# Optimization experiments

Hardware: AMD Instinct MI355X
Metric: run time of the kernel (lower is better)

Reference implementation:

```python
import jax, jax.numpy as jnp
import numpy as np

TAU = 2.0          # LIF membrane time constant (spikingjelly default)
ALPHA = 2.0        # ATan surrogate width
EPS = 1e-5         # BatchNorm eps
NUM_HEADS = 8
SCALE = 0.125

@jax.custom_vjp
def spike(x):
    return (x >= 0.0).astype(x.dtype)

def _spike_fwd(x):
    return (x >= 0.0).astype(x.dtype), x

def _spike_bwd(x, g):
    # ATan surrogate gradient (spikingjelly default)
    return (g * (ALPHA / 2.0) / (1.0 + (jnp.pi / 2.0 * ALPHA * x) ** 2),)

spike.defvjp(_spike_fwd, _spike_bwd)

def lif(x, v_th):
    # Multi-step LIF over leading time axis T; hard reset to 0, v_reset=0.
    def step(v, xt):
        h = v + (xt - v) / TAU
        s = spike(h - v_th)
        return h * (1.0 - s), s
    _, s = jax.lax.scan(step, jnp.zeros_like(x[0]), x)
    return s

def bn(x, g, b, m, v):
    # BatchNorm1d in eval mode over channel (last) dim
    return (x - m) * jax.lax.rsqrt(v + EPS) * g + b

def setup_inputs() -> dict:
    key = jax.random.key(0)
    ks = jax.random.split(key, 16)
    T, B, N, C = 4, 16, 512, 512
    s = 1.0 / np.sqrt(C)
    inp = {"x": jax.random.normal(ks[0], (T, B, N, C), jnp.float32)}
    for i, p in enumerate("qkvp"):
        inp[f"w{p}"] = jax.random.normal(ks[1 + i], (C, C), jnp.float32) * s
        inp[f"b{p}"] = jnp.zeros((C,), jnp.float32)
        inp[f"{p}_gamma"] = jnp.ones((C,), jnp.float32)
        inp[f"{p}_beta"] = jnp.zeros((C,), jnp.float32)
        inp[f"{p}_mean"] = jax.random.normal(ks[5 + i], (C,), jnp.float32) * 0.1
        inp[f"{p}_var"] = jax.random.uniform(ks[9 + i], (C,), jnp.float32, minval=0.5, maxval=1.5)
    return inp

def reference(x, wq, bq, q_gamma, q_beta, q_mean, q_var,
              wk, bk, k_gamma, k_beta, k_mean, k_var,
              wv, bv, v_gamma, v_beta, v_mean, v_var,
              wp, bp, p_gamma, p_beta, p_mean, p_var):
    T, B, N, C = x.shape
    H = NUM_HEADS
    D = C // H

    def branch(w, b, g, be, m, va):
        y = bn(x @ w.T + b, g, be, m, va)          # Linear -> BN1d (eval)
        y = lif(y, 1.0)                             # spiking activation
        return y.reshape(T, B, N, H, D).transpose(0, 1, 3, 2, 4)  # [T,B,H,N,D]

    q = branch(wq, bq, q_gamma, q_beta, q_mean, q_var)
    k = branch(wk, bk, k_gamma, k_beta, k_mean, k_var)
    v = branch(wv, bv, v_gamma, v_beta, v_mean, v_var)

    attn = jnp.einsum('tbhnd,tbhmd->tbhnm', q, k) * SCALE  # [T,B,H,N,N]
    o = jnp.einsum('tbhnm,tbhmd->tbhnd', attn, v)          # [T,B,H,N,D]
    o = o.transpose(0, 1, 3, 2, 4).reshape(T, B, N, C)
    o = lif(o, 0.5)                                        # attn_lif, v_th=0.5
    o = bn(o @ wp.T + bp, p_gamma, p_beta, p_mean, p_var)
    return lif(o, 1.0)
```

## Files before the change

### kernel.cpp

```cpp
#include <hip/hip_runtime.h>
#include <hip/hip_bf16.h>
#include <hip/hip_fp16.h>
#include <cstddef>
#include <cstdint>

#define T_ 4
#define B_ 16
#define N_ 512
#define C_ 512
#define H_ 8
#define D_ 64
#define BN_T (B_*N_)

typedef unsigned short u16;
typedef __attribute__((ext_vector_type(8))) short bf16x8;
typedef __attribute__((ext_vector_type(8))) _Float16 f16x8;
typedef __attribute__((ext_vector_type(8))) unsigned short u16x8;
typedef __attribute__((ext_vector_type(4))) float f32x4;

__device__ __forceinline__ u16 f2bf_exact(float f) {
    union { float f; unsigned u; } x; x.f = f; return (u16)(x.u >> 16);
}
__device__ __forceinline__ void split2(float f, u16& h1, u16& h2) {
    const __half a = __float2half(f);
    const float r = (f - __half2float(a)) * 2048.0f;
    const __half b = __float2half(r);
    h1 = __half_as_ushort(a); h2 = __half_as_ushort(b);
}
__device__ __forceinline__ int swz(int rr, int q) {
    return (rr << 6) + (((q ^ ((rr >> 1) & 3)) & 3) << 4);
}
__device__ __forceinline__ int SW(int row, int col) {
    return (row << 6) + (col ^ ((row & 7) << 3));
}
__device__ __forceinline__ void gload16(const void* g, void* l) {
    __builtin_amdgcn_global_load_lds(
        (const __attribute__((address_space(1))) unsigned int*)g,
        (__attribute__((address_space(3))) unsigned int*)l, 16, 0, 0);
}

__global__ __launch_bounds__(256) void k_split_x(
    const float* __restrict__ x, u16* __restrict__ x1t, u16* __restrict__ x2t)
{
    const int tile = blockIdx.x;
    const int mt = tile >> 4, kb = tile & 15;
    const int tid = threadIdx.x;
    const int rr = tid >> 1, kh = tid & 1;
    const int t = rr & 3, bn = mt * 32 + (rr >> 2);
    const float* src = x + ((size_t)t * BN_T + bn) * C_ + kb * 32 + kh * 16;
    float f[16];
    *reinterpret_cast<float4*>(f + 0)  = *reinterpret_cast<const float4*>(src + 0);
    *reinterpret_cast<float4*>(f + 4)  = *reinterpret_cast<const float4*>(src + 4);
    *reinterpret_cast<float4*>(f + 8)  = *reinterpret_cast<const float4*>(src + 8);
    *reinterpret_cast<float4*>(f + 12) = *reinterpret_cast<const float4*>(src + 12);
    char* d1 = (char*)(x1t + ((size_t)tile << 12));
    char* d2 = (char*)(x2t + ((size_t)tile << 12));
    #pragma unroll
    for (int j = 0; j < 2; ++j) {
        u16x8 p1, p2;
        #pragma unroll
        for (int e = 0; e < 8; ++e) { u16 h1, h2; split2(f[8*j+e], h1, h2); p1[e] = h1; p2[e] = h2; }
        const int q = 2 * kh + j;
        *reinterpret_cast<u16x8*>(d1 + swz(rr, q)) = p1;
        *reinterpret_cast<u16x8*>(d2 + swz(rr, q)) = p2;
    }
}

__global__ __launch_bounds__(256) void k_split_w(
    const float* __restrict__ w, u16* __restrict__ w1t, u16* __restrict__ w2t)
{
    const int tile = blockIdx.x;
    const int nt = tile >> 4, kb = tile & 15;
    const int tid = threadIdx.x;
    const int rr = tid >> 1, kh = tid & 1;
    const int c = nt * 128 + rr;
    const float* src = w + (size_t)c * C_ + kb * 32 + kh * 16;
    float f[16];
    *reinterpret_cast<float4*>(f + 0)  = *reinterpret_cast<const float4*>(src + 0);
    *reinterpret_cast<float4*>(f + 4)  = *reinterpret_cast<const float4*>(src + 4);
    *reinterpret_cast<float4*>(f + 8)  = *reinterpret_cast<const float4*>(src + 8);
    *reinterpret_cast<float4*>(f + 12) = *reinterpret_cast<const float4*>(src + 12);
    char* d1 = (char*)(w1t + ((size_t)tile << 12));
    char* d2 = (char*)(w2t + ((size_t)tile << 12));
    #pragma unroll
    for (int j = 0; j < 2; ++j) {
        u16x8 p1, p2;
        #pragma unroll
        for (int e = 0; e < 8; ++e) { u16 h1, h2; split2(f[8*j+e], h1, h2); p1[e] = h1; p2[e] = h2; }
        const int q = 2 * kh + j;
        *reinterpret_cast<u16x8*>(d1 + swz(rr, q)) = p1;
        *reinterpret_cast<u16x8*>(d2 + swz(rr, q)) = p2;
    }
}

__global__ __launch_bounds__(512, 2) void k_linear_qkv(
    const u16* __restrict__ a1t, const u16* __restrict__ a2t,
    const u16* __restrict__ wt_base,
    const float* __restrict__ bi0, const float* __restrict__ ga0, const float* __restrict__ be0,
    const float* __restrict__ mu0, const float* __restrict__ va0,
    const float* __restrict__ bi1, const float* __restrict__ ga1, const float* __restrict__ be1,
    const float* __restrict__ mu1, const float* __restrict__ va1,
    const float* __restrict__ bi2, const float* __restrict__ ga2, const float* __restrict__ be2,
    const float* __restrict__ mu2, const float* __restrict__ va2,
    u16* __restrict__ oq, u16* __restrict__ ok, u16* __restrict__ ov)
{
    __shared__ u16 lds[3][6][4096];

    const int dd  = blockIdx.x;
    const int lid = (dd & 7) * 192 + (dd >> 3);
    const int mt  = lid / 6;
    const int rem = lid - mt * 6;
    const int li  = rem >> 1;
    const int nt  = rem & 1;
    const int bn0 = mt * 32;
    const int c0  = nt * 256;

    const float* bias  = li == 0 ? bi0 : li == 1 ? bi1 : bi2;
    const float* gamma = li == 0 ? ga0 : li == 1 ? ga1 : ga2;
    const float* beta  = li == 0 ? be0 : li == 1 ? be1 : be2;
    const float* mean  = li == 0 ? mu0 : li == 1 ? mu1 : mu2;
    const float* var   = li == 0 ? va0 : li == 1 ? va1 : va2;
    u16* outp = li == 0 ? oq : li == 1 ? ok : ov;

    const size_t WSZ = (size_t)C_ * C_;
    const u16* w1t = wt_base + (size_t)(2 * li) * WSZ;
    const u16* w2t = wt_base + (size_t)(2 * li + 1) * WSZ;

    const int tid = threadIdx.x;
    const int wv  = tid >> 6, lane = tid & 63;
    const int l15 = lane & 15, g = (lane >> 4) & 3;
    const int wr  = wv >> 2, wc = wv & 3;
    const int so  = tid * 16;

    f32x4 accA[4][4], accB[4][4];
    #pragma unroll
    for (int rt = 0; rt < 4; ++rt)
        #pragma unroll
        for (int ct = 0; ct < 4; ++ct) { accA[rt][ct] = {0,0,0,0}; accB[rt][ct] = {0,0,0,0}; }

    const size_t abase  = (size_t)mt * 16;
    const size_t bbase0 = (size_t)(nt * 2 + 0) * 16;
    const size_t bbase1 = (size_t)(nt * 2 + 1) * 16;

    auto stage = [&](int buf, int kb) {
        char* L = (char*)&lds[buf][0][0];
        gload16((const char*)(a1t + ((abase  + kb) << 12)) + so, L + 0 * 8192 + so);
        gload16((const char*)(a2t + ((abase  + kb) << 12)) + so, L + 1 * 8192 + so);
        gload16((const char*)(w1t + ((bbase0 + kb) << 12)) + so, L + 2 * 8192 + so);
        gload16((const char*)(w1t + ((bbase1 + kb) << 12)) + so, L + 3 * 8192 + so);
        gload16((const char*)(w2t + ((bbase0 + kb) << 12)) + so, L + 4 * 8192 + so);
        gload16((const char*)(w2t + ((bbase1 + kb) << 12)) + so, L + 5 * 8192 + so);
    };
    auto comp = [&](int buf) {
        const char* L = (const char*)&lds[buf][0][0];
        f16x8 a1[4], a2[4];
        #pragma unroll
        for (int rt = 0; rt < 4; ++rt) {
            const int rr = 64 * wr + 16 * rt + l15;
            a1[rt] = *reinterpret_cast<const f16x8*>(L + 0 * 8192 + swz(rr, g));
            a2[rt] = *reinterpret_cast<const f16x8*>(L + 1 * 8192 + swz(rr, g));
        }
        __builtin_amdgcn_s_setprio(1);
        #pragma unroll
        for (int ct = 0; ct < 4; ++ct) {
            const int cc = 64 * wc + 16 * ct;
            const int ub = 2 + (cc >> 7);
            const int rrB = (cc & 127) + l15;
            const f16x8 b1 = *reinterpret_cast<const f16x8*>(L + ub * 8192 + swz(rrB, g));
            const f16x8 b2 = *reinterpret_cast<const f16x8*>(L + (ub + 2) * 8192 + swz(rrB, g));
            #pragma unroll
            for (int rt = 0; rt < 4; ++rt) {
                accA[rt][ct] = __builtin_amdgcn_mfma_f32_16x16x32_f16(a1[rt], b1, accA[rt][ct], 0, 0, 0);
                accB[rt][ct] = __builtin_amdgcn_mfma_f32_16x16x32_f16(a2[rt], b1, accB[rt][ct], 0, 0, 0);
                accB[rt][ct] = __builtin_amdgcn_mfma_f32_16x16x32_f16(a1[rt], b2, accB[rt][ct], 0, 0, 0);
            }
        }
        __builtin_amdgcn_s_setprio(0);
    };

    stage(0, 0);
    stage(1, 1);
    __builtin_amdgcn_sched_barrier(0);
    asm volatile("s_waitcnt vmcnt(6) lgkmcnt(0)" ::: "memory");
    __builtin_amdgcn_s_barrier();
    __builtin_amdgcn_sched_barrier(0);

    #pragma unroll 1
    for (int k = 0; k < 14; ++k) {
        stage((k + 2) % 3, k + 2);
        comp(k % 3);
        __builtin_amdgcn_sched_barrier(0);
        asm volatile("s_waitcnt vmcnt(6) lgkmcnt(0)" ::: "memory");
        __builtin_amdgcn_s_barrier();
        __builtin_amdgcn_sched_barrier(0);
    }
    comp(14 % 3);
    __builtin_amdgcn_sched_barrier(0);
    asm volatile("s_waitcnt vmcnt(0) lgkmcnt(0)" ::: "memory");
    __builtin_amdgcn_s_barrier();
    __builtin_amdgcn_sched_barrier(0);
    comp(15 % 3);

    #pragma unroll
    for (int ct = 0; ct < 4; ++ct) {
        const int c = c0 + 64 * wc + 16 * ct + l15;
        const float rs = 1.0f / sqrtf(var[c] + 1e-5f);
        const float ga = gamma[c], be = beta[c], mu = mean[c], bi = bias[c];
        #pragma unroll
        for (int rt = 0; rt < 4; ++rt) {
            const int bn = bn0 + 16 * wr + 4 * rt + g;
            float vm = 0.f;
            #pragma unroll
            for (int r = 0; r < 4; ++r) {
                const float y = accA[rt][ct][r] + accB[rt][ct][r] * (1.0f / 2048.0f) + bi;
                const float ybn = (y - mu) * rs * ga + be;
                const float h = vm + (ybn - vm) * 0.5f;
                const bool sp = (h >= 1.0f);
                vm = sp ? 0.f : h;
                const int b = bn >> 9, n = bn & 511;
                const int hh = c >> 6, d2 = c & 63;
                outp[((((size_t)r * B_ + b) * H_ + hh) * N_ + n) * D_ + d2] = sp ? 0x3F80 : 0;
            }
        }
    }
}

__global__ __launch_bounds__(512, 2) void k_linear_out(
    const u16* __restrict__ a1t,
    const u16* __restrict__ w1t, const u16* __restrict__ w2t,
    const float* __restrict__ bias, const float* __restrict__ gamma,
    const float* __restrict__ beta, const float* __restrict__ mean,
    const float* __restrict__ var, float* __restrict__ outp)
{
    __shared__ u16 lds[3][5][4096];

    const int dd  = blockIdx.x;
    const int lid = (dd & 7) * 64 + (dd >> 3);
    const int mt  = lid >> 1;
    const int nt  = lid & 1;
    const int bn0 = mt * 32;
    const int c0  = nt * 256;

    const int tid = threadIdx.x;
    const int wv  = tid >> 6, lane = tid & 63;
    const int l15 = lane & 15, g = (lane >> 4) & 3;
    const int wr  = wv >> 2, wc = wv & 3;
    const int so  = tid * 16;

    f32x4 accA[4][4], accB[4][4];
    #pragma unroll
    for (int rt = 0; rt < 4; ++rt)
        #pragma unroll
        for (int ct = 0; ct < 4; ++ct) { accA[rt][ct] = {0,0,0,0}; accB[rt][ct] = {0,0,0,0}; }

    const size_t abase  = (size_t)mt * 16;
    const size_t bbase0 = (size_t)(nt * 2 + 0) * 16;
    const size_t bbase1 = (size_t)(nt * 2 + 1) * 16;

    auto stage = [&](int buf, int kb) {
        char* L = (char*)&lds[buf][0][0];
        gload16((const char*)(a1t + ((abase  + kb) << 12)) + so, L + 0 * 8192 + so);
        gload16((const char*)(w1t + ((bbase0 + kb) << 12)) + so, L + 1 * 8192 + so);
        gload16((const char*)(w1t + ((bbase1 + kb) << 12)) + so, L + 2 * 8192 + so);
        gload16((const char*)(w2t + ((bbase0 + kb) << 12)) + so, L + 3 * 8192 + so);
        gload16((const char*)(w2t + ((bbase1 + kb) << 12)) + so, L + 4 * 8192 + so);
    };
    auto comp = [&](int buf) {
        const char* L = (const char*)&lds[buf][0][0];
        f16x8 a1[4];
        #pragma unroll
        for (int rt = 0; rt < 4; ++rt) {
            const int rr = 64 * wr + 16 * rt + l15;
            a1[rt] = *reinterpret_cast<const f16x8*>(L + 0 * 8192 + swz(rr, g));
        }
        __builtin_amdgcn_s_setprio(1);
        #pragma unroll
        for (int ct = 0; ct < 4; ++ct) {
            const int cc = 64 * wc + 16 * ct;
            const int ub = 1 + (cc >> 7);
            const int rrB = (cc & 127) + l15;
            const f16x8 b1 = *reinterpret_cast<const f16x8*>(L + ub * 8192 + swz(rrB, g));
            const f16x8 b2 = *reinterpret_cast<const f16x8*>(L + (ub + 2) * 8192 + swz(rrB, g));
            #pragma unroll
            for (int rt = 0; rt < 4; ++rt) {
                accA[rt][ct] = __builtin_amdgcn_mfma_f32_16x16x32_f16(a1[rt], b1, accA[rt][ct], 0, 0, 0);
                accB[rt][ct] = __builtin_amdgcn_mfma_f32_16x16x32_f16(a1[rt], b2, accB[rt][ct], 0, 0, 0);
            }
        }
        __builtin_amdgcn_s_setprio(0);
    };

    stage(0, 0);
    stage(1, 1);
    __builtin_amdgcn_sched_barrier(0);
    asm volatile("s_waitcnt vmcnt(5) lgkmcnt(0)" ::: "memory");
    __builtin_amdgcn_s_barrier();
    __builtin_amdgcn_sched_barrier(0);

    #pragma unroll 1
    for (int k = 0; k < 14; ++k) {
        stage((k + 2) % 3, k + 2);
        comp(k % 3);
        __builtin_amdgcn_sched_barrier(0);
        asm volatile("s_waitcnt vmcnt(5) lgkmcnt(0)" ::: "memory");
        __builtin_amdgcn_s_barrier();
        __builtin_amdgcn_sched_barrier(0);
    }
    comp(14 % 3);
    __builtin_amdgcn_sched_barrier(0);
    asm volatile("s_waitcnt vmcnt(0) lgkmcnt(0)" ::: "memory");
    __builtin_amdgcn_s_barrier();
    __builtin_amdgcn_sched_barrier(0);
    comp(15 % 3);

    #pragma unroll
    for (int ct = 0; ct < 4; ++ct) {
        const int c = c0 + 64 * wc + 16 * ct + l15;
        const float rs = 1.0f / sqrtf(var[c] + 1e-5f);
        const float ga = gamma[c], be = beta[c], mu = mean[c], bi = bias[c];
        #pragma unroll
        for (int rt = 0; rt < 4; ++rt) {
            const int bn = bn0 + 16 * wr + 4 * rt + g;
            float vm = 0.f;
            #pragma unroll
            for (int r = 0; r < 4; ++r) {
                const float y = accA[rt][ct][r] + accB[rt][ct][r] * (1.0f / 2048.0f) + bi;
                const float ybn = (y - mu) * rs * ga + be;
                const float h = vm + (ybn - vm) * 0.5f;
                const bool sp = (h >= 1.0f);
                vm = sp ? 0.f : h;
                outp[((size_t)r * BN_T + bn) * C_ + c] = sp ? 1.0f : 0.0f;
            }
        }
    }
}

__global__ __launch_bounds__(512, 2) void k_attn_mfma(
    const u16* __restrict__ qg, const u16* __restrict__ kg,
    const u16* __restrict__ vg, u16* __restrict__ s2t)
{
    __shared__ u16 kf[8][4096];
    __shared__ u16 vf[8][4096];
    __shared__ u16 ssb[8][1024];

    const int id  = blockIdx.x;
    const int lid = (id & 7) * 64 + (id >> 3);
    const int bh  = lid >> 2;
    const int qt  = lid & 3;
    const int b   = bh >> 3, hh = bh & 7;

    const int tid  = threadIdx.x;
    const int w    = tid >> 6, lane = tid & 63;
    const int l15  = lane & 15, g = lane >> 4;

    const int vkv = (tid & 15) * 4;
    const int vd  = ((tid >> 4) & 15) * 4;

    bf16x8 qa[2];
    f32x4 vmem[4], oacc[4];
    #pragma unroll
    for (int d0 = 0; d0 < 4; ++d0) { vmem[d0] = {0,0,0,0}; oacc[d0] = {0,0,0,0}; }

    #pragma unroll 1
    for (int t = 0; t < T_; ++t) {
        const size_t base = ((size_t)t * (B_ * H_) + bh) * (size_t)(N_ * D_);
        if (t > 0) __syncthreads();

        {
            const size_t qrow = base + (size_t)(qt * 128 + 16 * w + l15) * D_;
            qa[0] = *reinterpret_cast<const bf16x8*>(qg + qrow + 8 * g);
            qa[1] = *reinterpret_cast<const bf16x8*>(qg + qrow + 32 + 8 * g);
        }
        {
            const u16* kb = kg + base;
            #pragma unroll
            for (int i = 0; i < 8; ++i) {
                const int r64 = tid >> 3;
                const int col = (tid & 7) * 8;
                const u16x8 v = *reinterpret_cast<const u16x8*>(kb + ((size_t)(tid + 512 * i)) * 8);
                *reinterpret_cast<u16x8*>(&kf[i][SW(r64, col)]) = v;
            }
        }
        {
            const u16* vb = vg + base;
            #pragma unroll
            for (int i = 0; i < 4; ++i) {
                const int jt = 2 * i + (tid >> 8);
                const int m0 = jt * 64;
                ushort4 r0 = *reinterpret_cast<const ushort4*>(vb + (size_t)(m0 + vkv + 0) * D_ + vd);
                ushort4 r1 = *reinterpret_cast<const ushort4*>(vb + (size_t)(m0 + vkv + 1) * D_ + vd);
                ushort4 r2 = *reinterpret_cast<const ushort4*>(vb + (size_t)(m0 + vkv + 2) * D_ + vd);
                ushort4 r3 = *reinterpret_cast<const ushort4*>(vb + (size_t)(m0 + vkv + 3) * D_ + vd);
                ushort4 wv4;
                wv4.x = r0.x; wv4.y = r1.x; wv4.z = r2.x; wv4.w = r3.x;
                *reinterpret_cast<ushort4*>(&vf[jt][SW(vd + 0, vkv)]) = wv4;
                wv4.x = r0.y; wv4.y = r1.y; wv4.z = r2.y; wv4.w = r3.y;
                *reinterpret_cast<ushort4*>(&vf[jt][SW(vd + 1, vkv)]) = wv4;
                wv4.x = r0.z; wv4.y = r1.z; wv4.z = r2.z; wv4.w = r3.z;
                *reinterpret_cast<ushort4*>(&vf[jt][SW(vd + 2, vkv)]) = wv4;
                wv4.x = r0.w; wv4.y = r1.w; wv4.z = r2.w; wv4.w = r3.w;
                *reinterpret_cast<ushort4*>(&vf[jt][SW(vd + 3, vkv)]) = wv4;
            }
        }
        __syncthreads();

        u16* sb = &ssb[w][0];
        #pragma unroll
        for (int jt = 0; jt < 8; ++jt) {
            __builtin_amdgcn_s_setprio(1);
            #pragma unroll
            for (int kvt = 0; kvt < 2; ++kvt) {
                f32x4 acc = {0.f, 0.f, 0.f, 0.f};
                #pragma unroll
                for (int c = 0; c < 2; ++c) {
                    const bf16x8 kb = *reinterpret_cast<const bf16x8*>(
                        &kf[jt][SW(16 * kvt + l15, 32 * c + 8 * g)]);
                    acc = __builtin_amdgcn_mfma_f32_16x16x32_bf16(qa[c], kb, acc, 0, 0, 0);
                }
                #pragma unroll
                for (int r = 0; r < 4; ++r)
                    sb[SW(4 * g + r, 16 * kvt + l15)] = f2bf_exact(acc[r]);
            }
            {
                const bf16x8 sa = *reinterpret_cast<const bf16x8*>(&sb[SW(l15, 8 * g)]);
                #pragma unroll
                for (int d0 = 0; d0 < 4; ++d0) {
                    const bf16x8 vb2 = *reinterpret_cast<const bf16x8*>(
                        &vf[jt][SW(16 * d0 + l15, 8 * g)]);
                    oacc[d0] = __builtin_amdgcn_mfma_f32_16x16x32_bf16(sa, vb2, oacc[d0], 0, 0, 0);
                }
            }
            #pragma unroll
            for (int kvt = 2; kvt < 4; ++kvt) {
                f32x4 acc = {0.f, 0.f, 0.f, 0.f};
                #pragma unroll
                for (int c = 0; c < 2; ++c) {
                    const bf16x8 kb = *reinterpret_cast<const bf16x8*>(
                        &kf[jt][SW(16 * kvt + l15, 32 * c + 8 * g)]);
                    acc = __builtin_amdgcn_mfma_f32_16x16x32_bf16(qa[c], kb, acc, 0, 0, 0);
                }
                #pragma unroll
                for (int r = 0; r < 4; ++r)
                    sb[SW(4 * g + r, 16 * kvt + l15)] = f2bf_exact(acc[r]);
            }
            {
                const bf16x8 sa = *reinterpret_cast<const bf16x8*>(&sb[SW(l15, 32 + 8 * g)]);
                #pragma unroll
                for (int d0 = 0; d0 < 4; ++d0) {
                    const bf16x8 vb2 = *reinterpret_cast<const bf16x8*>(
                        &vf[jt][SW(16 * d0 + l15, 32 + 8 * g)]);
                    oacc[d0] = __builtin_amdgcn_mfma_f32_16x16x32_bf16(sa, vb2, oacc[d0], 0, 0, 0);
                }
            }
            __builtin_amdgcn_s_setprio(0);
        }

        #pragma unroll
        for (int d0 = 0; d0 < 4; ++d0) {
            const int c = hh * 64 + d0 * 16 + l15;
            const int kb2 = c >> 5, kq = (c >> 3) & 3, e = c & 7;
            #pragma unroll
            for (int r = 0; r < 4; ++r) {
                const float o = oacc[d0][r] * 0.125f;
                const float h = vmem[d0][r] + (o - vmem[d0][r]) * 0.5f;
                const bool sp = (h >= 0.5f);
                vmem[d0][r] = sp ? 0.f : h;
                const int n = qt * 128 + 16 * w + 4 * g + r;
                const int bn = b * 512 + n;
                const int mt2 = bn >> 5;
                const int rr2 = (bn & 31) * 4 + t;
                const size_t off = (((size_t)mt2 * 16 + kb2) << 13) + (rr2 << 6)
                                 + (((kq ^ ((rr2 >> 1) & 3)) & 3) << 4) + (e << 1);
                *(u16*)((char*)s2t + off) = sp ? 0x3C00 : 0;
            }
            oacc[d0] = {0.f, 0.f, 0.f, 0.f};
        }
    }
}

extern "C" void kernel_launch(void* const* d_in, const int* in_sizes, int n_in,
                              void* d_out, int out_size, void* d_ws, size_t ws_size,
                              hipStream_t stream)
{
    const float* x = (const float*)d_in[0];
    const float* W[4]  = {(const float*)d_in[1],  (const float*)d_in[7],  (const float*)d_in[13], (const float*)d_in[19]};
    const float* Bi[4] = {(const float*)d_in[2],  (const float*)d_in[8],  (const float*)d_in[14], (const float*)d_in[20]};
    const float* Ga[4] = {(const float*)d_in[3],  (const float*)d_in[9],  (const float*)d_in[15], (const float*)d_in[21]};
    const float* Be[4] = {(const float*)d_in[4],  (const float*)d_in[10], (const float*)d_in[16], (const float*)d_in[22]};
    const float* Mu[4] = {(const float*)d_in[5],  (const float*)d_in[11], (const float*)d_in[17], (const float*)d_in[23]};
    const float* Va[4] = {(const float*)d_in[6],  (const float*)d_in[12], (const float*)d_in[18], (const float*)d_in[24]};

    const size_t SPK = (size_t)T_ * B_ * N_ * C_;
    const size_t WSZ = (size_t)C_ * C_;
    u16* qb  = (u16*)d_ws;
    u16* kbf = qb + SPK;
    u16* vbf = kbf + SPK;
    u16* x1t = vbf + SPK;
    u16* x2t = x1t + SPK;
    u16* wt  = x2t + SPK;
    u16* s2t = x1t;

    dim3 blk(256);
    k_split_x<<<4096, blk, 0, stream>>>(x, x1t, x2t);
    for (int i = 0; i < 4; ++i)
        k_split_w<<<64, blk, 0, stream>>>(W[i], wt + (2*i) * WSZ, wt + (2*i+1) * WSZ);

    k_linear_qkv<<<1536, dim3(512), 0, stream>>>(x1t, x2t, wt,
        Bi[0], Ga[0], Be[0], Mu[0], Va[0],
        Bi[1], Ga[1], Be[1], Mu[1], Va[1],
        Bi[2], Ga[2], Be[2], Mu[2], Va[2],
        qb, kbf, vbf);
    k_attn_mfma<<<512, dim3(512), 0, stream>>>(qb, kbf, vbf, s2t);
    k_linear_out<<<512, dim3(512), 0, stream>>>(s2t, wt + 6*WSZ, wt + 7*WSZ,
        Bi[3], Ga[3], Be[3], Mu[3], Va[3], (float*)d_out);
}
```

Baseline: 300.7 us.

## Split GEMM main loop into four phases interleaving staged loads with MFMA groups

Restructures the two split-fp16 GEMM kernels' K loops so each iteration runs as four phases, one per output column tile. Each phase issues a slice of the next-next stage's global-to-LDS loads, reads its B fragments, synchronises with a workgroup barrier and then runs its MFMA group. The aim is to spread memory issue across compute and overlap LDS reads with MFMA in the style of a ping-pong schedule. The cost is many more s_barrier calls per iteration, which could add synchronisation stalls.

```diff
diff --git a/kernel.cpp b/kernel.cpp
--- a/kernel.cpp
+++ b/kernel.cpp
@@ -38,6 +38,51 @@
         (const __attribute__((address_space(1))) unsigned int*)g,
         (__attribute__((address_space(3))) unsigned int*)l, 16, 0, 0);
 }
+
+#define PHASE3T(p, STAGE, WAIT) do {                                          \
+    const int cc_ = 64 * wc + 16 * (p);                                       \
+    const int rrB_ = (cc_ & 127) + l15;                                       \
+    const char* LB_ = L + (2 + (cc_ >> 7)) * 8192;                            \
+    const f16x8 b1_ = *reinterpret_cast<const f16x8*>(LB_ + swz(rrB_, g));    \
+    const f16x8 b2_ = *reinterpret_cast<const f16x8*>(LB_ + 16384 + swz(rrB_, g)); \
+    STAGE;                                                                    \
+    WAIT;                                                                     \
+    __builtin_amdgcn_sched_barrier(0);                                        \
+    __builtin_amdgcn_s_barrier();                                             \
+    asm volatile("s_waitcnt lgkmcnt(0)" ::: "memory");                        \
+    __builtin_amdgcn_sched_barrier(0);                                        \
+    __builtin_amdgcn_s_setprio(1);                                            \
+    _Pragma("unroll")                                                         \
+    for (int rt_ = 0; rt_ < 4; ++rt_) {                                       \
+        accA[rt_][p] = __builtin_amdgcn_mfma_f32_16x16x32_f16(a1[rt_], b1_, accA[rt_][p], 0, 0, 0); \
+        accB[rt_][p] = __builtin_amdgcn_mfma_f32_16x16x32_f16(a2[rt_], b1_, accB[rt_][p], 0, 0, 0); \
+        accB[rt_][p] = __builtin_amdgcn_mfma_f32_16x16x32_f16(a1[rt_], b2_, accB[rt_][p], 0, 0, 0); \
+    }                                                                         \
+    __builtin_amdgcn_s_setprio(0);                                            \
+    __builtin_amdgcn_s_barrier();                                             \
+} while (0)
+
+#define PHASE2T(p, STAGE, WAIT) do {                                          \
+    const int cc_ = 64 * wc + 16 * (p);                                       \
+    const int rrB_ = (cc_ & 127) + l15;                                       \
+    const char* LB_ = L + (1 + (cc_ >> 7)) * 8192;                            \
+    const f16x8 b1_ = *reinterpret_cast<const f16x8*>(LB_ + swz(rrB_, g));    \
+    const f16x8 b2_ = *reinterpret_cast<const f16x8*>(LB_ + 16384 + swz(rrB_, g)); \
+    STAGE;                                                                    \
+    WAIT;                                                                     \
+    __builtin_amdgcn_sched_barrier(0);                                        \
+    __builtin_amdgcn_s_barrier();                                             \
+    asm volatile("s_waitcnt lgkmcnt(0)" ::: "memory");                        \
+    __builtin_amdgcn_sched_barrier(0);                                        \
+    __builtin_amdgcn_s_setprio(1);                                            \
+    _Pragma("unroll")                                                         \
+    for (int rt_ = 0; rt_ < 4; ++rt_) {                                       \
+        accA[rt_][p] = __builtin_amdgcn_mfma_f32_16x16x32_f16(a1[rt_], b1_, accA[rt_][p], 0, 0, 0); \
+        accB[rt_][p] = __builtin_amdgcn_mfma_f32_16x16x32_f16(a1[rt_], b2_, accB[rt_][p], 0, 0, 0); \
+    }                                                                         \
+    __builtin_amdgcn_s_setprio(0);                                            \
+    __builtin_amdgcn_s_barrier();                                             \
+} while (0)
 
 __global__ __launch_bounds__(256) void k_split_x(
     const float* __restrict__ x, u16* __restrict__ x1t, u16* __restrict__ x2t)
@@ -141,65 +186,42 @@
     const size_t abase  = (size_t)mt * 16;
     const size_t bbase0 = (size_t)(nt * 2 + 0) * 16;
     const size_t bbase1 = (size_t)(nt * 2 + 1) * 16;
-
-    auto stage = [&](int buf, int kb) {
-        char* L = (char*)&lds[buf][0][0];
-        gload16((const char*)(a1t + ((abase  + kb) << 12)) + so, L + 0 * 8192 + so);
-        gload16((const char*)(a2t + ((abase  + kb) << 12)) + so, L + 1 * 8192 + so);
-        gload16((const char*)(w1t + ((bbase0 + kb) << 12)) + so, L + 2 * 8192 + so);
-        gload16((const char*)(w1t + ((bbase1 + kb) << 12)) + so, L + 3 * 8192 + so);
-        gload16((const char*)(w2t + ((bbase0 + kb) << 12)) + so, L + 4 * 8192 + so);
-        gload16((const char*)(w2t + ((bbase1 + kb) << 12)) + so, L + 5 * 8192 + so);
-    };
-    auto comp = [&](int buf) {
-        const char* L = (const char*)&lds[buf][0][0];
+    char* const L0 = (char*)&lds[0][0][0];
+
+    auto sA = [&](int kb) { char* Ls = L0 + (kb % 3) * 49152;
+        gload16((const char*)(a1t + ((abase  + kb) << 12)) + so, Ls + 0 * 8192 + so);
+        gload16((const char*)(a2t + ((abase  + kb) << 12)) + so, Ls + 1 * 8192 + so); };
+    auto sB1 = [&](int kb) { char* Ls = L0 + (kb % 3) * 49152;
+        gload16((const char*)(w1t + ((bbase0 + kb) << 12)) + so, Ls + 2 * 8192 + so);
+        gload16((const char*)(w1t + ((bbase1 + kb) << 12)) + so, Ls + 3 * 8192 + so); };
+    auto sB2 = [&](int kb) { char* Ls = L0 + (kb % 3) * 49152;
+        gload16((const char*)(w2t + ((bbase0 + kb) << 12)) + so, Ls + 4 * 8192 + so);
+        gload16((const char*)(w2t + ((bbase1 + kb) << 12)) + so, Ls + 5 * 8192 + so); };
+
+    sA(0); sB1(0); sB2(0);
+    sA(1); sB1(1); sB2(1);
+    __builtin_amdgcn_sched_barrier(0);
+    asm volatile("s_waitcnt vmcnt(6)" ::: "memory");
+    __builtin_amdgcn_s_barrier();
+    __builtin_amdgcn_sched_barrier(0);
+
+    #pragma unroll 1
+    for (int k = 0; k < 16; ++k) {
+        const char* L = L0 + (k % 3) * 49152;
         f16x8 a1[4], a2[4];
         #pragma unroll
         for (int rt = 0; rt < 4; ++rt) {
             const int rr = 64 * wr + 16 * rt + l15;
-            a1[rt] = *reinterpret_cast<const f16x8*>(L + 0 * 8192 + swz(rr, g));
-            a2[rt] = *reinterpret_cast<const f16x8*>(L + 1 * 8192 + swz(rr, g));
-        }
-        __builtin_amdgcn_s_setprio(1);
-        #pragma unroll
-        for (int ct = 0; ct < 4; ++ct) {
-            const int cc = 64 * wc + 16 * ct;
-            const int ub = 2 + (cc >> 7);
-            const int rrB = (cc & 127) + l15;
-            const f16x8 b1 = *reinterpret_cast<const f16x8*>(L + ub * 8192 + swz(rrB, g));
-            const f16x8 b2 = *reinterpret_cast<const f16x8*>(L + (ub + 2) * 8192 + swz(rrB, g));
-            #pragma unroll
-            for (int rt = 0; rt < 4; ++rt) {
-                accA[rt][ct] = __builtin_amdgcn_mfma_f32_16x16x32_f16(a1[rt], b1, accA[rt][ct], 0, 0, 0);
-                accB[rt][ct] = __builtin_amdgcn_mfma_f32_16x16x32_f16(a2[rt], b1, accB[rt][ct], 0, 0, 0);
-                accB[rt][ct] = __builtin_amdgcn_mfma_f32_16x16x32_f16(a1[rt], b2, accB[rt][ct], 0, 0, 0);
-            }
-        }
-        __builtin_amdgcn_s_setprio(0);
-    };
-
-    stage(0, 0);
-    stage(1, 1);
-    __builtin_amdgcn_sched_barrier(0);
-    asm volatile("s_waitcnt vmcnt(6) lgkmcnt(0)" ::: "memory");
-    __builtin_amdgcn_s_barrier();
-    __builtin_amdgcn_sched_barrier(0);
-
-    #pragma unroll 1
-    for (int k = 0; k < 14; ++k) {
-        stage((k + 2) % 3, k + 2);
-        comp(k % 3);
-        __builtin_amdgcn_sched_barrier(0);
-        asm volatile("s_waitcnt vmcnt(6) lgkmcnt(0)" ::: "memory");
-        __builtin_amdgcn_s_barrier();
-        __builtin_amdgcn_sched_barrier(0);
-    }
-    comp(14 % 3);
-    __builtin_amdgcn_sched_barrier(0);
-    asm volatile("s_waitcnt vmcnt(0) lgkmcnt(0)" ::: "memory");
-    __builtin_amdgcn_s_barrier();
-    __builtin_amdgcn_sched_barrier(0);
-    comp(15 % 3);
+            a1[rt] = *reinterpret_cast<const f16x8*>(L + swz(rr, g));
+            a2[rt] = *reinterpret_cast<const f16x8*>(L + 8192 + swz(rr, g));
+        }
+        const bool st = (k <= 13);
+        PHASE3T(0, if (st) sA(k + 2), );
+        PHASE3T(1, if (st) sB1(k + 2), );
+        PHASE3T(2, if (st) sB2(k + 2), );
+        if (k < 14) { PHASE3T(3, , asm volatile("s_waitcnt vmcnt(6)" ::: "memory")); }
+        else        { PHASE3T(3, , asm volatile("s_waitcnt vmcnt(0)" ::: "memory")); }
+    }
 
     #pragma unroll
     for (int ct = 0; ct < 4; ++ct) {
@@ -256,62 +278,40 @@
     const size_t abase  = (size_t)mt * 16;
     const size_t bbase0 = (size_t)(nt * 2 + 0) * 16;
     const size_t bbase1 = (size_t)(nt * 2 + 1) * 16;
-
-    auto stage = [&](int buf, int kb) {
-        char* L = (char*)&lds[buf][0][0];
-        gload16((const char*)(a1t + ((abase  + kb) << 12)) + so, L + 0 * 8192 + so);
-        gload16((const char*)(w1t + ((bbase0 + kb) << 12)) + so, L + 1 * 8192 + so);
-        gload16((const char*)(w1t + ((bbase1 + kb) << 12)) + so, L + 2 * 8192 + so);
-        gload16((const char*)(w2t + ((bbase0 + kb) << 12)) + so, L + 3 * 8192 + so);
-        gload16((const char*)(w2t + ((bbase1 + kb) << 12)) + so, L + 4 * 8192 + so);
-    };
-    auto comp = [&](int buf) {
-        const char* L = (const char*)&lds[buf][0][0];
+    char* const L0 = (char*)&lds[0][0][0];
+
+    auto s0 = [&](int kb) { char* Ls = L0 + (kb % 3) * 40960;
+        gload16((const char*)(a1t + ((abase  + kb) << 12)) + so, Ls + 0 * 8192 + so);
+        gload16((const char*)(w1t + ((bbase0 + kb) << 12)) + so, Ls + 1 * 8192 + so); };
+    auto s1 = [&](int kb) { char* Ls = L0 + (kb % 3) * 40960;
+        gload16((const char*)(w1t + ((bbase1 + kb) << 12)) + so, Ls + 2 * 8192 + so);
+        gload16((const char*)(w2t + ((bbase0 + kb) << 12)) + so, Ls + 3 * 8192 + so); };
+    auto s2 = [&](int kb) { char* Ls = L0 + (kb % 3) * 40960;
+        gload16((const char*)(w2t + ((bbase1 + kb) << 12)) + so, Ls + 4 * 8192 + so); };
+
+    s0(0); s1(0); s2(0);
+    s0(1); s1(1); s2(1);
+    __builtin_amdgcn_sched_barrier(0);
+    asm volatile("s_waitcnt vmcnt(5)" ::: "memory");
+    __builtin_amdgcn_s_barrier();
+    __builtin_amdgcn_sched_barrier(0);
+
+    #pragma unroll 1
+    for (int k = 0; k < 16; ++k) {
+        const char* L = L0 + (k % 3) * 40960;
         f16x8 a1[4];
         #pragma unroll
         for (int rt = 0; rt < 4; ++rt) {
             const int rr = 64 * wr + 16 * rt + l15;
-            a1[rt] = *reinterpret_cast<const f16x8*>(L + 0 * 8192 + swz(rr, g));
-        }
-        __builtin_amdgcn_s_setprio(1);
-        #pragma unroll
-        for (int ct = 0; ct < 4; ++ct) {
-            const int cc = 64 * wc + 16 * ct;
-            const int ub = 1 + (cc >> 7);
-            const int rrB = (cc & 127) + l15;
-            const f16x8 b1 = *reinterpret_cast<const f16x8*>(L + ub * 8192 + swz(rrB, g));
-            const f16x8 b2 = *reinterpret_cast<const f16x8*>(L + (ub + 2) * 8192 + swz(rrB, g));
-            #pragma unroll
-            for (int rt = 0; rt < 4; ++rt) {
-                accA[rt][ct] = __builtin_amdgcn_mfma_f32_16x16x32_f16(a1[rt], b1, accA[rt][ct], 0, 0, 0);
-                accB[rt][ct] = __builtin_amdgcn_mfma_f32_16x16x32_f16(a1[rt], b2, accB[rt][ct], 0, 0, 0);
-            }
-        }
-        __builtin_amdgcn_s_setprio(0);
-    };
-
-    stage(0, 0);
-    stage(1, 1);
-    __builtin_amdgcn_sched_barrier(0);
-    asm volatile("s_waitcnt vmcnt(5) lgkmcnt(0)" ::: "memory");
-    __builtin_amdgcn_s_barrier();
-    __builtin_amdgcn_sched_barrier(0);
-
-    #pragma unroll 1
-    for (int k = 0; k < 14; ++k) {
-        stage((k + 2) % 3, k + 2);
-        comp(k % 3);
-        __builtin_amdgcn_sched_barrier(0);
-        asm volatile("s_waitcnt vmcnt(5) lgkmcnt(0)" ::: "memory");
-        __builtin_amdgcn_s_barrier();
-        __builtin_amdgcn_sched_barrier(0);
-    }
-    comp(14 % 3);
-    __builtin_amdgcn_sched_barrier(0);
-    asm volatile("s_waitcnt vmcnt(0) lgkmcnt(0)" ::: "memory");
-    __builtin_amdgcn_s_barrier();
-    __builtin_amdgcn_sched_barrier(0);
-    comp(15 % 3);
+            a1[rt] = *reinterpret_cast<const f16x8*>(L + swz(rr, g));
+        }
+        const bool st = (k <= 13);
+        PHASE2T(0, if (st) s0(k + 2), );
+        PHASE2T(1, if (st) s1(k + 2), );
+        PHASE2T(2, if (st) s2(k + 2), );
+        if (k < 14) { PHASE2T(3, , asm volatile("s_waitcnt vmcnt(5)" ::: "memory")); }
+        else        { PHASE2T(3, , asm volatile("s_waitcnt vmcnt(0)" ::: "memory")); }
+    }
 
     #pragma unroll
     for (int ct = 0; ct < 4; ++ct) {
```

After: 322.5 us. 7.2% more time.
